# Kernel optimization log

Hardware: AMD Instinct MI355X
Metric: run time of the kernel (lower is better)

## Reference

```python
import jax, jax.numpy as jnp
import numpy as np

N_NODES = 100000
N_EDGES = 1600000
F_IN = 500
HIDDEN = 64
N_CLASS = 40


def gcn_conv(x, W, b, src, dst, n_nodes):
    """PyG GCNConv: add self-loops, symmetric deg^-1/2 normalization,
    linear transform then scatter-add aggregation at dst."""
    h = x @ W  # [N, out]
    loop = jnp.arange(n_nodes, dtype=src.dtype)
    s = jnp.concatenate([src, loop])  # sources incl. self-loops
    d = jnp.concatenate([dst, loop])
    deg = jax.ops.segment_sum(jnp.ones_like(d, dtype=h.dtype), d, num_segments=n_nodes)
    dinv = jnp.where(deg > 0, jax.lax.rsqrt(deg), 0.0)
    norm = dinv[s] * dinv[d]  # [E+N]
    msg = h[s] * norm[:, None]  # gather + scale, [E+N, out]
    out = jax.ops.segment_sum(msg, d, num_segments=n_nodes)
    return out + b


def setup_inputs() -> dict:
    key = jax.random.key(0)
    k1, k2, k3, k4 = jax.random.split(key, 4)
    x = jax.random.normal(k1, (N_NODES, F_IN), dtype=jnp.float32)
    edge_index = jax.random.randint(k2, (2, N_EDGES), 0, N_NODES, dtype=jnp.int64)
    # Glorot-style init for GCNConv weights
    W1 = jax.random.normal(k3, (F_IN, HIDDEN), dtype=jnp.float32) / np.sqrt(F_IN)
    b1 = jnp.zeros((HIDDEN,), dtype=jnp.float32)
    W2 = jax.random.normal(k4, (HIDDEN, N_CLASS), dtype=jnp.float32) / np.sqrt(HIDDEN)
    b2 = jnp.zeros((N_CLASS,), dtype=jnp.float32)
    return {"x": x, "W1": W1, "b1": b1, "W2": W2, "b2": b2, "edge_index": edge_index}


def reference(x, W1, b1, W2, b2, edge_index):
    src, dst = edge_index[0], edge_index[1]
    n = x.shape[0]
    h = jax.nn.relu(gcn_conv(x, W1, b1, src, dst, n))
    # dropout is identity in eval mode (F.dropout with training=False)
    out = gcn_conv(h, W2, b2, src, dst, n)
    return jax.nn.log_softmax(out, axis=1)
```

## Files before the change

### kernel.cpp

```cpp
#include <hip/hip_runtime.h>
#include <math.h>

#define N_NODES 100000
#define N_EDGES 1600000
#define F_IN    500
#define HIDDEN  64
#define N_CLASS 40
#define KPAD    512

#define NB   2048
#define NPB  49
#define EPB  16384
#define CAP  1536

typedef __attribute__((ext_vector_type(4))) float f32x4;
typedef __attribute__((ext_vector_type(8))) __bf16 bf16x8;

__device__ __forceinline__ unsigned short f2bf(float f) {
    unsigned int u = __float_as_uint(f);
    u = (u + 0x7FFF + ((u >> 16) & 1)) >> 16;
    return (unsigned short)u;
}
__device__ __forceinline__ float bfu_lo(unsigned int v) {
    return __uint_as_float(v << 16);
}
__device__ __forceinline__ float bfu_hi(unsigned int v) {
    return __uint_as_float(v & 0xFFFF0000u);
}

__global__ void k_zero_int(int* p, int n) {
    int i = blockIdx.x * blockDim.x + threadIdx.x;
    if (i < n) p[i] = 0;
}

__global__ void k_prep_w1t(const float* __restrict__ w1, unsigned short* __restrict__ w1t) {
    int idx = blockIdx.x * blockDim.x + threadIdx.x;
    if (idx >= HIDDEN * KPAD) return;
    int n = idx >> 9, k = idx & (KPAD - 1);
    float v = (k < F_IN) ? w1[k * HIDDEN + n] : 0.f;
    w1t[idx] = f2bf(v);
}

__launch_bounds__(1024)
__global__ void k_bhist(const int* __restrict__ dst, int* __restrict__ bcnt, int e) {
    __shared__ int h[NB];
    for (int i = threadIdx.x; i < NB; i += 1024) h[i] = 0;
    __syncthreads();
    int base = blockIdx.x * EPB;
#pragma unroll
    for (int j = 0; j < 16; ++j) {
        int i = base + j * 1024 + threadIdx.x;
        if (i < e) atomicAdd(&h[dst[i] / NPB], 1);
    }
    __syncthreads();
    for (int i = threadIdx.x; i < NB; i += 1024)
        if (h[i]) atomicAdd(&bcnt[i], h[i]);
}

__launch_bounds__(1024)
__global__ void k_bscan(const int* __restrict__ bcnt, int* __restrict__ bptr,
                        int* __restrict__ bcur) {
    __shared__ int s[1024];
    int t = threadIdx.x;
    int a = bcnt[2 * t], b = bcnt[2 * t + 1];
    int v = a + b;
    s[t] = v;
    __syncthreads();
    for (int off = 1; off < 1024; off <<= 1) {
        int u = (t >= off) ? s[t - off] : 0;
        __syncthreads();
        s[t] += u;
        __syncthreads();
    }
    int excl = s[t] - v;
    bptr[2 * t] = excl;     bptr[2 * t + 1] = excl + a;
    bcur[2 * t] = excl;     bcur[2 * t + 1] = excl + a;
    if (t == 1023) bptr[NB] = s[1023];
}

__launch_bounds__(1024)
__global__ void k_bfill(const int* __restrict__ src, const int* __restrict__ dst,
                        int* __restrict__ bcur, int2* __restrict__ ebuf, int e) {
    __shared__ int hist[NB];
    __shared__ int base_[NB];
    for (int i = threadIdx.x; i < NB; i += 1024) hist[i] = 0;
    __syncthreads();
    int b0 = blockIdx.x * EPB;
    int s_[16], d_[16];
#pragma unroll
    for (int j = 0; j < 16; ++j) {
        int i = b0 + j * 1024 + threadIdx.x;
        if (i < e) {
            s_[j] = src[i];
            d_[j] = dst[i];
            atomicAdd(&hist[d_[j] / NPB], 1);
        } else d_[j] = -1;
    }
    __syncthreads();
    for (int i = threadIdx.x; i < NB; i += 1024) {
        int hc = hist[i];
        base_[i] = hc ? atomicAdd(&bcur[i], hc) : 0;
        hist[i] = 0;
    }
    __syncthreads();
#pragma unroll
    for (int j = 0; j < 16; ++j) {
        if (d_[j] >= 0) {
            int bu = d_[j] / NPB;
            int r = atomicAdd(&hist[bu], 1);
            ebuf[base_[bu] + r] = make_int2(s_[j], d_[j]);
        }
    }
}

__launch_bounds__(256)
__global__ void k_bucket_csr(const int2* __restrict__ ebuf, const int* __restrict__ bptr,
                             int* __restrict__ rp, int* __restrict__ col,
                             float* __restrict__ dinv, int n) {
    int b  = blockIdx.x;
    int lo = b * NPB;
    if (lo >= n) return;
    int hi  = min(lo + NPB, n);
    int eb0 = bptr[b], ec = bptr[b + 1] - eb0;

    __shared__ int2 pairs[CAP];
    __shared__ int  hist[NPB];
    __shared__ int  excl[NPB + 1];
    for (int j = threadIdx.x; j < NPB; j += 256) hist[j] = 0;
    __syncthreads();
    for (int i = threadIdx.x; i < ec; i += 256) {
        int2 p = ebuf[eb0 + i];
        if (i < CAP) pairs[i] = p;
        atomicAdd(&hist[p.y - lo], 1);
    }
    __syncthreads();
    if (threadIdx.x == 0) {
        int acc = 0;
        for (int j = 0; j < NPB; ++j) { excl[j] = acc; acc += hist[j]; }
        excl[NPB] = acc;
    }
    __syncthreads();
    for (int j = threadIdx.x; j < hi - lo; j += 256) {
        rp[lo + j]   = eb0 + excl[j];
        dinv[lo + j] = rsqrtf((float)(hist[j] + 1));
    }
    if (hi == n && threadIdx.x == 0) rp[n] = eb0 + ec;
    __syncthreads();
    for (int j = threadIdx.x; j < NPB; j += 256) hist[j] = 0;
    __syncthreads();
    for (int i = threadIdx.x; i < ec; i += 256) {
        int2 p  = (i < CAP) ? pairs[i] : ebuf[eb0 + i];
        int  li = p.y - lo;
        int  r  = atomicAdd(&hist[li], 1);
        col[eb0 + excl[li] + r] = p.x;
    }
}

__launch_bounds__(256)
__global__ void k_gemm1(const float* __restrict__ x, const unsigned short* __restrict__ w1t,
                        const float* __restrict__ dinv, unsigned short* __restrict__ hs, int n) {
    __shared__ unsigned short xs[4][32][40];
    const int tid  = threadIdx.x;
    const int wave = tid >> 6;
    const int lane = tid & 63;
    const int quad = lane >> 4;
    const int l16  = lane & 15;
    const int rowb = blockIdx.x * 128 + wave * 32;

    const int srow = lane >> 3;
    const int skof = (lane & 7) * 4;

    f32x4 acc[2][4];
#pragma unroll
    for (int rt = 0; rt < 2; ++rt)
#pragma unroll
        for (int ct = 0; ct < 4; ++ct) acc[rt][ct] = (f32x4)0.f;

    for (int ks = 0; ks < 16; ++ks) {
        const int k0 = ks * 32;

        float4 tmp[4];
        if (ks < 15) {
#pragma unroll
            for (int u = 0; u < 4; ++u) {
                int grow = rowb + u * 8 + srow;
                tmp[u] = (grow < n) ? *(const float4*)&x[(size_t)grow * F_IN + k0 + skof]
                                    : make_float4(0.f, 0.f, 0.f, 0.f);
            }
        } else {
#pragma unroll
            for (int u = 0; u < 4; ++u) {
                int grow = rowb + u * 8 + srow;
                const float* p = &x[(size_t)grow * F_IN];
                float v0 = (grow < n && k0 + skof + 0 < F_IN) ? p[k0 + skof + 0] : 0.f;
                float v1 = (grow < n && k0 + skof + 1 < F_IN) ? p[k0 + skof + 1] : 0.f;
                float v2 = (grow < n && k0 + skof + 2 < F_IN) ? p[k0 + skof + 2] : 0.f;
                float v3 = (grow < n && k0 + skof + 3 < F_IN) ? p[k0 + skof + 3] : 0.f;
                tmp[u] = make_float4(v0, v1, v2, v3);
            }
        }
        bf16x8 bfrag[4];
#pragma unroll
        for (int ct = 0; ct < 4; ++ct)
            bfrag[ct] = *(const bf16x8*)&w1t[(ct * 16 + l16) * KPAD + k0 + quad * 8];

#pragma unroll
        for (int u = 0; u < 4; ++u) {
            unsigned int lo = (unsigned int)f2bf(tmp[u].x) | ((unsigned int)f2bf(tmp[u].y) << 16);
            unsigned int hi = (unsigned int)f2bf(tmp[u].z) | ((unsigned int)f2bf(tmp[u].w) << 16);
            *(uint2*)&xs[wave][u * 8 + srow][skof] = make_uint2(lo, hi);
        }
        __syncthreads();

        union { bf16x8 v; unsigned int u[4]; } af[2];
#pragma unroll
        for (int rt = 0; rt < 2; ++rt) {
            uint2 a = *(const uint2*)&xs[wave][rt * 16 + l16][quad * 8];
            uint2 b = *(const uint2*)&xs[wave][rt * 16 + l16][quad * 8 + 4];
            af[rt].u[0] = a.x; af[rt].u[1] = a.y; af[rt].u[2] = b.x; af[rt].u[3] = b.y;
        }
#pragma unroll
        for (int rt = 0; rt < 2; ++rt)
#pragma unroll
            for (int ct = 0; ct < 4; ++ct)
                acc[rt][ct] = __builtin_amdgcn_mfma_f32_16x16x32_bf16(
                    af[rt].v, bfrag[ct], acc[rt][ct], 0, 0, 0);
        __syncthreads();
    }

#pragma unroll
    for (int rt = 0; rt < 2; ++rt) {
#pragma unroll
        for (int reg = 0; reg < 4; ++reg) {
            int grow = rowb + rt * 16 + quad * 4 + reg;
            if (grow < n) {
                float dv = dinv[grow];
#pragma unroll
                for (int ct = 0; ct < 4; ++ct)
                    hs[(size_t)grow * HIDDEN + ct * 16 + l16] = f2bf(dv * acc[rt][ct][reg]);
            }
        }
    }
}

template <int F, bool RELU, bool LSM>
__global__ void k_agg(const unsigned int* __restrict__ hs, const int* __restrict__ rp,
                      const int* __restrict__ col, const float* __restrict__ dinv,
                      const float* __restrict__ bias, float* __restrict__ out, int n) {
    constexpr int PW = F / 2;
    int wid  = (blockIdx.x * blockDim.x + threadIdx.x) >> 6;
    wid = __builtin_amdgcn_readfirstlane(wid);
    if (wid >= n) return;
    const int lane = threadIdx.x & 63;
    const int half = lane >> 5;
    const int p    = lane & 31;
    const bool act = p < PW;

    int beg = rp[wid], end = rp[wid + 1];
    float alo = 0.f, ahi = 0.f;
    int e = beg + half;
    for (; e + 6 < end; e += 8) {
        int c0 = col[e], c1 = col[e + 2], c2 = col[e + 4], c3 = col[e + 6];
        unsigned v0 = act ? hs[(unsigned)c0 * PW + p] : 0u;
        unsigned v1 = act ? hs[(unsigned)c1 * PW + p] : 0u;
        unsigned v2 = act ? hs[(unsigned)c2 * PW + p] : 0u;
        unsigned v3 = act ? hs[(unsigned)c3 * PW + p] : 0u;
        alo += bfu_lo(v0) + bfu_lo(v1) + bfu_lo(v2) + bfu_lo(v3);
        ahi += bfu_hi(v0) + bfu_hi(v1) + bfu_hi(v2) + bfu_hi(v3);
    }
    for (; e < end; e += 2) {
        int c0 = col[e];
        unsigned v0 = act ? hs[(unsigned)c0 * PW + p] : 0u;
        alo += bfu_lo(v0);
        ahi += bfu_hi(v0);
    }
    alo += __shfl_xor(alo, 32);
    ahi += __shfl_xor(ahi, 32);

    float di = dinv[wid];
    unsigned sv = act ? hs[(unsigned)wid * PW + p] : 0u;
    float2 bv = act ? *(const float2*)&bias[2 * p] : make_float2(0.f, 0.f);
    float rlo = di * (alo + bfu_lo(sv)) + bv.x;
    float rhi = di * (ahi + bfu_hi(sv)) + bv.y;
    if (RELU) { rlo = fmaxf(rlo, 0.f); rhi = fmaxf(rhi, 0.f); }
    if (LSM) {
        float m = act ? fmaxf(rlo, rhi) : -INFINITY;
#pragma unroll
        for (int off = 16; off; off >>= 1) m = fmaxf(m, __shfl_xor(m, off));
        float ex = act ? (__expf(rlo - m) + __expf(rhi - m)) : 0.f;
#pragma unroll
        for (int off = 16; off; off >>= 1) ex += __shfl_xor(ex, off);
        float lse = m + __logf(ex);
        rlo -= lse; rhi -= lse;
    }
    if (half == 0 && act)
        *(float2*)&out[(size_t)wid * F + 2 * p] = make_float2(rlo, rhi);
}

__launch_bounds__(256)
__global__ void k_gemm2(const float* __restrict__ a, const float* __restrict__ w,
                        const float* __restrict__ dinv, unsigned short* __restrict__ out, int n) {
    __shared__ float ws[HIDDEN * N_CLASS];
    for (int idx = threadIdx.x; idx < HIDDEN * N_CLASS; idx += 256) ws[idx] = w[idx];
    __syncthreads();
    int idx = blockIdx.x * 256 + threadIdx.x;
    if (idx >= n * N_CLASS) return;
    int i = idx / N_CLASS, j = idx - i * N_CLASS;
    float s = 0.f;
#pragma unroll
    for (int k = 0; k < HIDDEN; k += 4) {
        float4 xv = *(const float4*)&a[(size_t)i * HIDDEN + k];
        s = fmaf(xv.x, ws[k * N_CLASS + j], s);
        s = fmaf(xv.y, ws[(k + 1) * N_CLASS + j], s);
        s = fmaf(xv.z, ws[(k + 2) * N_CLASS + j], s);
        s = fmaf(xv.w, ws[(k + 3) * N_CLASS + j], s);
    }
    out[idx] = f2bf(dinv[i] * s);
}

extern "C" void kernel_launch(void* const* d_in, const int* in_sizes, int n_in,
                              void* d_out, int out_size, void* d_ws, size_t ws_size,
                              hipStream_t stream) {
    const float* x   = (const float*)d_in[0];
    const float* W1  = (const float*)d_in[1];
    const float* b1  = (const float*)d_in[2];
    const float* W2  = (const float*)d_in[3];
    const float* b2  = (const float*)d_in[4];
    const int*   ei  = (const int*)d_in[5];
    const int*   src = ei;
    const int*   dst = ei + N_EDGES;
    float*       out = (float*)d_out;

    char*  ws  = (char*)d_ws;
    size_t off = 0;
    auto alloc = [&](size_t bytes) -> void* {
        void* p = ws + off;
        off += (bytes + 255) & ~(size_t)255;
        return p;
    };
    int*            bcnt = (int*)alloc((size_t)NB * 4);
    int*            bptr = (int*)alloc((size_t)(NB + 1) * 4);
    int*            bcur = (int*)alloc((size_t)NB * 4);
    int*            rp   = (int*)alloc((size_t)(N_NODES + 1) * 4);
    int*            col  = (int*)alloc((size_t)N_EDGES * 4);
    float*          dinv = (float*)alloc((size_t)N_NODES * 4);
    unsigned short* w1t  = (unsigned short*)alloc((size_t)HIDDEN * KPAD * 2);
    unsigned short* h1s  = (unsigned short*)alloc((size_t)N_NODES * HIDDEN * 2);
    float*          h1a  = (float*)alloc((size_t)N_NODES * HIDDEN * 4);
    int2*           ebuf = (int2*)h1a;
    unsigned short* h2s  = h1s;

    const int NBH = (N_EDGES + EPB - 1) / EPB;

    k_zero_int<<<(NB + 255) / 256, 256, 0, stream>>>(bcnt, NB);
    k_prep_w1t<<<(HIDDEN * KPAD + 255) / 256, 256, 0, stream>>>(W1, w1t);
    k_bhist<<<NBH, 1024, 0, stream>>>(dst, bcnt, N_EDGES);
    k_bscan<<<1, 1024, 0, stream>>>(bcnt, bptr, bcur);
    k_bfill<<<NBH, 1024, 0, stream>>>(src, dst, bcur, ebuf, N_EDGES);
    k_bucket_csr<<<NB, 256, 0, stream>>>(ebuf, bptr, rp, col, dinv, N_NODES);

    k_gemm1<<<(N_NODES + 127) / 128, 256, 0, stream>>>(x, w1t, dinv, h1s, N_NODES);
    k_agg<HIDDEN, true, false><<<(N_NODES + 3) / 4, 256, 0, stream>>>(
        (const unsigned int*)h1s, rp, col, dinv, b1, h1a, N_NODES);

    k_gemm2<<<(N_NODES * N_CLASS + 255) / 256, 256, 0, stream>>>(h1a, W2, dinv, h2s, N_NODES);
    k_agg<N_CLASS, false, true><<<(N_NODES + 3) / 4, 256, 0, stream>>>(
        (const unsigned int*)h2s, rp, col, dinv, b2, out, N_NODES);
}
```

Baseline: 538.7 us.

## Widen aggregation gathers to 8-byte loads with four edge lanes and persistent grid

The aggregation kernel now has each lane load four bf16 features (uint2) instead of two, so 16 lanes cover a row and a wavefront processes four edges at once, reduced with two shuffle rounds. It switches to a grid-stride persistent loop with a fixed 2048-block grid and launch bounds. Separately, the bucket-count zeroing is folded into the weight-prep kernel to drop one launch. The aim is more memory-level parallelism per wavefront and less launch overhead. The cost is more shuffle reductions and lanes left idle for the 40-class layer.

Result: faster. 497.7 us (-7.6%).

```diff
diff --git a/kernel.cpp b/kernel.cpp
--- a/kernel.cpp
+++ b/kernel.cpp
@@ -28,13 +28,10 @@
     return __uint_as_float(v & 0xFFFF0000u);
 }
 
-__global__ void k_zero_int(int* p, int n) {
-    int i = blockIdx.x * blockDim.x + threadIdx.x;
-    if (i < n) p[i] = 0;
-}
-
-__global__ void k_prep_w1t(const float* __restrict__ w1, unsigned short* __restrict__ w1t) {
+__global__ void k_prep_w1t(const float* __restrict__ w1, unsigned short* __restrict__ w1t,
+                           int* __restrict__ bcnt) {
     int idx = blockIdx.x * blockDim.x + threadIdx.x;
+    if (idx < NB) bcnt[idx] = 0;
     if (idx >= HIDDEN * KPAD) return;
     int n = idx >> 9, k = idx & (KPAD - 1);
     float v = (k < F_IN) ? w1[k * HIDDEN + n] : 0.f;
@@ -244,57 +241,79 @@
 }
 
 template <int F, bool RELU, bool LSM>
-__global__ void k_agg(const unsigned int* __restrict__ hs, const int* __restrict__ rp,
+__launch_bounds__(256)
+__global__ void k_agg(const uint2* __restrict__ hs2, const int* __restrict__ rp,
                       const int* __restrict__ col, const float* __restrict__ dinv,
                       const float* __restrict__ bias, float* __restrict__ out, int n) {
-    constexpr int PW = F / 2;
-    int wid  = (blockIdx.x * blockDim.x + threadIdx.x) >> 6;
-    wid = __builtin_amdgcn_readfirstlane(wid);
-    if (wid >= n) return;
+    constexpr int PW2 = F / 4;
     const int lane = threadIdx.x & 63;
-    const int half = lane >> 5;
-    const int p    = lane & 31;
-    const bool act = p < PW;
-
-    int beg = rp[wid], end = rp[wid + 1];
-    float alo = 0.f, ahi = 0.f;
-    int e = beg + half;
-    for (; e + 6 < end; e += 8) {
-        int c0 = col[e], c1 = col[e + 2], c2 = col[e + 4], c3 = col[e + 6];
-        unsigned v0 = act ? hs[(unsigned)c0 * PW + p] : 0u;
-        unsigned v1 = act ? hs[(unsigned)c1 * PW + p] : 0u;
-        unsigned v2 = act ? hs[(unsigned)c2 * PW + p] : 0u;
-        unsigned v3 = act ? hs[(unsigned)c3 * PW + p] : 0u;
-        alo += bfu_lo(v0) + bfu_lo(v1) + bfu_lo(v2) + bfu_lo(v3);
-        ahi += bfu_hi(v0) + bfu_hi(v1) + bfu_hi(v2) + bfu_hi(v3);
-    }
-    for (; e < end; e += 2) {
-        int c0 = col[e];
-        unsigned v0 = act ? hs[(unsigned)c0 * PW + p] : 0u;
-        alo += bfu_lo(v0);
-        ahi += bfu_hi(v0);
-    }
-    alo += __shfl_xor(alo, 32);
-    ahi += __shfl_xor(ahi, 32);
-
-    float di = dinv[wid];
-    unsigned sv = act ? hs[(unsigned)wid * PW + p] : 0u;
-    float2 bv = act ? *(const float2*)&bias[2 * p] : make_float2(0.f, 0.f);
-    float rlo = di * (alo + bfu_lo(sv)) + bv.x;
-    float rhi = di * (ahi + bfu_hi(sv)) + bv.y;
-    if (RELU) { rlo = fmaxf(rlo, 0.f); rhi = fmaxf(rhi, 0.f); }
-    if (LSM) {
-        float m = act ? fmaxf(rlo, rhi) : -INFINITY;
-#pragma unroll
-        for (int off = 16; off; off >>= 1) m = fmaxf(m, __shfl_xor(m, off));
-        float ex = act ? (__expf(rlo - m) + __expf(rhi - m)) : 0.f;
-#pragma unroll
-        for (int off = 16; off; off >>= 1) ex += __shfl_xor(ex, off);
-        float lse = m + __logf(ex);
-        rlo -= lse; rhi -= lse;
-    }
-    if (half == 0 && act)
-        *(float2*)&out[(size_t)wid * F + 2 * p] = make_float2(rlo, rhi);
+    const int q    = lane >> 4;
+    const int p    = lane & 15;
+    const bool act = p < PW2;
+    int wid = __builtin_amdgcn_readfirstlane((blockIdx.x * blockDim.x + threadIdx.x) >> 6);
+    const int nw = (gridDim.x * blockDim.x) >> 6;
+
+    for (; wid < n; wid += nw) {
+        const int beg = rp[wid], end = rp[wid + 1];
+        float a0 = 0.f, a1 = 0.f, a2 = 0.f, a3 = 0.f;
+        int e = beg + q;
+        for (; e + 12 < end; e += 16) {
+            int c0 = col[e], c1 = col[e + 4], c2 = col[e + 8], c3 = col[e + 12];
+            uint2 v0 = act ? hs2[(unsigned)c0 * PW2 + p] : make_uint2(0u, 0u);
+            uint2 v1 = act ? hs2[(unsigned)c1 * PW2 + p] : make_uint2(0u, 0u);
+            uint2 v2 = act ? hs2[(unsigned)c2 * PW2 + p] : make_uint2(0u, 0u);
+            uint2 v3 = act ? hs2[(unsigned)c3 * PW2 + p] : make_uint2(0u, 0u);
+            a0 += bfu_lo(v0.x) + bfu_lo(v1.x) + bfu_lo(v2.x) + bfu_lo(v3.x);
+            a1 += bfu_hi(v0.x) + bfu_hi(v1.x) + bfu_hi(v2.x) + bfu_hi(v3.x);
+            a2 += bfu_lo(v0.y) + bfu_lo(v1.y) + bfu_lo(v2.y) + bfu_lo(v3.y);
+            a3 += bfu_hi(v0.y) + bfu_hi(v1.y) + bfu_hi(v2.y) + bfu_hi(v3.y);
+        }
+        if (e + 4 < end) {
+            int c0 = col[e], c1 = col[e + 4];
+            uint2 v0 = act ? hs2[(unsigned)c0 * PW2 + p] : make_uint2(0u, 0u);
+            uint2 v1 = act ? hs2[(unsigned)c1 * PW2 + p] : make_uint2(0u, 0u);
+            a0 += bfu_lo(v0.x) + bfu_lo(v1.x);
+            a1 += bfu_hi(v0.x) + bfu_hi(v1.x);
+            a2 += bfu_lo(v0.y) + bfu_lo(v1.y);
+            a3 += bfu_hi(v0.y) + bfu_hi(v1.y);
+            e += 8;
+        }
+        if (e < end) {
+            int c0 = col[e];
+            uint2 v0 = act ? hs2[(unsigned)c0 * PW2 + p] : make_uint2(0u, 0u);
+            a0 += bfu_lo(v0.x); a1 += bfu_hi(v0.x);
+            a2 += bfu_lo(v0.y); a3 += bfu_hi(v0.y);
+        }
+        a0 += __shfl_xor(a0, 16); a1 += __shfl_xor(a1, 16);
+        a2 += __shfl_xor(a2, 16); a3 += __shfl_xor(a3, 16);
+        a0 += __shfl_xor(a0, 32); a1 += __shfl_xor(a1, 32);
+        a2 += __shfl_xor(a2, 32); a3 += __shfl_xor(a3, 32);
+
+        const float di = dinv[wid];
+        uint2 sv  = act ? hs2[(unsigned)wid * PW2 + p] : make_uint2(0u, 0u);
+        float4 bv = act ? *(const float4*)&bias[4 * p] : make_float4(0.f, 0.f, 0.f, 0.f);
+        float r0 = di * (a0 + bfu_lo(sv.x)) + bv.x;
+        float r1 = di * (a1 + bfu_hi(sv.x)) + bv.y;
+        float r2 = di * (a2 + bfu_lo(sv.y)) + bv.z;
+        float r3 = di * (a3 + bfu_hi(sv.y)) + bv.w;
+        if (RELU) {
+            r0 = fmaxf(r0, 0.f); r1 = fmaxf(r1, 0.f);
+            r2 = fmaxf(r2, 0.f); r3 = fmaxf(r3, 0.f);
+        }
+        if (LSM) {
+            float m = act ? fmaxf(fmaxf(r0, r1), fmaxf(r2, r3)) : -INFINITY;
+#pragma unroll
+            for (int off = 8; off; off >>= 1) m = fmaxf(m, __shfl_xor(m, off));
+            float ex = act ? (__expf(r0 - m) + __expf(r1 - m) + __expf(r2 - m) + __expf(r3 - m))
+                           : 0.f;
+#pragma unroll
+            for (int off = 8; off; off >>= 1) ex += __shfl_xor(ex, off);
+            float lse = m + __logf(ex);
+            r0 -= lse; r1 -= lse; r2 -= lse; r3 -= lse;
+        }
+        if (q == 0 && act)
+            *(float4*)&out[(size_t)wid * F + 4 * p] = make_float4(r0, r1, r2, r3);
+    }
 }
 
 __launch_bounds__(256)
@@ -352,18 +371,17 @@
 
     const int NBH = (N_EDGES + EPB - 1) / EPB;
 
-    k_zero_int<<<(NB + 255) / 256, 256, 0, stream>>>(bcnt, NB);
-    k_prep_w1t<<<(HIDDEN * KPAD + 255) / 256, 256, 0, stream>>>(W1, w1t);
+    k_prep_w1t<<<(HIDDEN * KPAD + 255) / 256, 256, 0, stream>>>(W1, w1t, bcnt);
     k_bhist<<<NBH, 1024, 0, stream>>>(dst, bcnt, N_EDGES);
     k_bscan<<<1, 1024, 0, stream>>>(bcnt, bptr, bcur);
     k_bfill<<<NBH, 1024, 0, stream>>>(src, dst, bcur, ebuf, N_EDGES);
     k_bucket_csr<<<NB, 256, 0, stream>>>(ebuf, bptr, rp, col, dinv, N_NODES);
 
     k_gemm1<<<(N_NODES + 127) / 128, 256, 0, stream>>>(x, w1t, dinv, h1s, N_NODES);
-    k_agg<HIDDEN, true, false><<<(N_NODES + 3) / 4, 256, 0, stream>>>(
-        (const unsigned int*)h1s, rp, col, dinv, b1, h1a, N_NODES);
+    k_agg<HIDDEN, true, false><<<2048, 256, 0, stream>>>(
+        (const uint2*)h1s, rp, col, dinv, b1, h1a, N_NODES);
 
     k_gemm2<<<(N_NODES * N_CLASS + 255) / 256, 256, 0, stream>>>(h1a, W2, dinv, h2s, N_NODES);
-    k_agg<N_CLASS, false, true><<<(N_NODES + 3) / 4, 256, 0, stream>>>(
-        (const unsigned int*)h2s, rp, col, dinv, b2, out, N_NODES);
-}
+    k_agg<N_CLASS, false, true><<<2048, 256, 0, stream>>>(
+        (const uint2*)h2s, rp, col, dinv, b2, out, N_NODES);
+}
```
